# Optimization experiments

Measured on AMD Instinct MI355X. Metric: run time of the kernel, lower is better.

## Reference

```python
import jax, jax.numpy as jnp
import numpy as np

NEG_INF = -1e30


def setup_inputs() -> dict:
    key = jax.random.key(0)
    x = jax.random.normal(key, (8192, 128), dtype=jnp.float32)
    return {"x": x, "k": 16}


def reference(x, k):
    # L2-normalize rows (cosine geometry), matching x / x.norm(p=2, dim=1)
    xn = x / jnp.linalg.norm(x, axis=1, keepdims=True)
    # All-pairs similarity S[i, j] = x_i . x_j  -> [N, N]
    S = jnp.matmul(xn, xn.T)
    # Denominator in the original includes ALL entries (self included):
    # log(exp(S[i,j]) / sum_m exp(S[i,m])) = S[i,j] - logsumexp_m S[i,m]
    lse = jax.nn.logsumexp(S, axis=1)  # [N]
    # BallTree on L2-normalized vectors orders neighbors by cosine similarity;
    # query(k+1) then dropping column 0 (self) == top-k of S with diagonal masked.
    n = S.shape[0]
    S_masked = jnp.where(jnp.eye(n, dtype=bool), NEG_INF, S)
    top_vals, _ = jax.lax.top_k(S_masked, k)  # [N, k]
    # loss = -sum_i sum_{j in kNN(i)} log(exp(S_ij)/denom_i)
    loss = -jnp.sum(top_vals - lse[:, None])
    return loss
```

## Files before the change

kernel.cpp:

```cpp
#include <hip/hip_runtime.h>
#include <math.h>

#define N 8192
#define D 128
#define KSEL 16
#define CH 512
#define NC (N / CH)
#define BM 128
#define PH 8
#define CPC 4
#define NEG_INF_F (-1e30f)
#define LOG2E 1.44269504f
#define LN2 0.69314718f

typedef __attribute__((ext_vector_type(8))) short short8;
typedef __attribute__((ext_vector_type(4))) float f32x4;
typedef __attribute__((ext_vector_type(2))) unsigned short ush2;

static __device__ __forceinline__ unsigned short f2bf(float f) {
    unsigned u = __float_as_uint(f);
    u += 0x7FFF + ((u >> 16) & 1);
    return (unsigned short)(u >> 16);
}

static __device__ __forceinline__ float exp2_raw(float x) {
    float r;
    asm("v_exp_f32 %0, %1" : "=v"(r) : "v"(x));
    return r;
}

#define GLOAD_LDS(gsrc, ldst)                                                     \
    __builtin_amdgcn_global_load_lds(                                             \
        (const __attribute__((address_space(1))) unsigned int*)(const void*)(gsrc),\
        (__attribute__((address_space(3))) unsigned int*)(void*)(ldst), 16, 0, 0)

__global__ void k_normalize(const float* __restrict__ x,
                            unsigned short* __restrict__ xnA,
                            unsigned short* __restrict__ xnB,
                            float* __restrict__ out) {
    if (blockIdx.x == 0 && threadIdx.x == 0) out[0] = 0.f;
    int row = blockIdx.x * 4 + (threadIdx.x >> 6);
    int lane = threadIdx.x & 63;
    const float2* x2 = (const float2*)(x + (size_t)row * D);
    float2 a = x2[lane];
    float s = fmaf(a.x, a.x, a.y * a.y);
#pragma unroll
    for (int off = 32; off > 0; off >>= 1) s += __shfl_xor(s, off, 64);
    float inv = rsqrtf(s);
    ush2 hb, ha;
    hb.x = f2bf(a.x * inv);
    hb.y = f2bf(a.y * inv);
    ha.x = f2bf(a.x * inv * LOG2E);
    ha.y = f2bf(a.y * inv * LOG2E);
    *(ush2*)(xnB + (size_t)row * D + lane * 2) = hb;
    *(ush2*)(xnA + (size_t)row * D + lane * 2) = ha;
}

__global__ __launch_bounds__(256, 4) void k_tiles(const unsigned short* __restrict__ xnA,
                                                  const unsigned short* __restrict__ xnB,
                                                  float* __restrict__ cs,
                                                  float* __restrict__ ct) {
    __shared__ unsigned short Bsh[2][4][4][64][8];

    const int tid = threadIdx.x;
    const int w = tid >> 6;
    const int l = tid & 63;
    const int r = l & 15;
    const int p = l >> 4;
    const int i0 = blockIdx.x * BM;
    const int j0 = blockIdx.y * CH;
    const int by = blockIdx.y;

    const unsigned short* ap = xnA + (size_t)(i0 + w * 16 + r) * D + p * 8;
    short8 af0 = *(const short8*)(ap);
    short8 af1 = *(const short8*)(ap + 32);
    short8 af2 = *(const short8*)(ap + 64);
    short8 af3 = *(const short8*)(ap + 96);
    const unsigned short* gp = ap + (size_t)64 * D;
    short8 ag0 = *(const short8*)(gp);
    short8 ag1 = *(const short8*)(gp + 32);
    short8 ag2 = *(const short8*)(gp + 64);
    short8 ag3 = *(const short8*)(gp + 96);

    float sE[2][4], c0[2][4], c1[2][4];
#pragma unroll
    for (int s2 = 0; s2 < 2; ++s2)
#pragma unroll
        for (int q = 0; q < 4; ++q) {
            sE[s2][q] = 0.f;
            c0[s2][q] = c1[s2][q] = NEG_INF_F;
        }

    const unsigned short* sbase = xnB + (size_t)(j0 + r) * D + p * 8 + w * 32;

#pragma unroll
    for (int tt = 0; tt < 4; ++tt)
        GLOAD_LDS(sbase + (size_t)tt * (16 * D), &Bsh[0][tt][w][0][0]);
    __syncthreads();

    for (int ph = 0; ph < PH; ++ph) {
        const int buf = ph & 1;
        if (ph < PH - 1) {
            const unsigned short* s1 = sbase + (size_t)(ph + 1) * (64 * D);
#pragma unroll
            for (int tt = 0; tt < 4; ++tt)
                GLOAD_LDS(s1 + (size_t)tt * (16 * D), &Bsh[buf ^ 1][tt][w][0][0]);
        }
#pragma unroll
        for (int tt = 0; tt < 4; ++tt) {
            short8 b0 = *(const short8*)&Bsh[buf][tt][0][l][0];
            short8 b1 = *(const short8*)&Bsh[buf][tt][1][l][0];
            short8 b2 = *(const short8*)&Bsh[buf][tt][2][l][0];
            short8 b3 = *(const short8*)&Bsh[buf][tt][3][l][0];
            f32x4 a0 = {0.f, 0.f, 0.f, 0.f};
            f32x4 a1 = {0.f, 0.f, 0.f, 0.f};
            a0 = __builtin_amdgcn_mfma_f32_16x16x32_bf16(af0, b0, a0, 0, 0, 0);
            a0 = __builtin_amdgcn_mfma_f32_16x16x32_bf16(af1, b1, a0, 0, 0, 0);
            a0 = __builtin_amdgcn_mfma_f32_16x16x32_bf16(af2, b2, a0, 0, 0, 0);
            a0 = __builtin_amdgcn_mfma_f32_16x16x32_bf16(af3, b3, a0, 0, 0, 0);
            a1 = __builtin_amdgcn_mfma_f32_16x16x32_bf16(ag0, b0, a1, 0, 0, 0);
            a1 = __builtin_amdgcn_mfma_f32_16x16x32_bf16(ag1, b1, a1, 0, 0, 0);
            a1 = __builtin_amdgcn_mfma_f32_16x16x32_bf16(ag2, b2, a1, 0, 0, 0);
            a1 = __builtin_amdgcn_mfma_f32_16x16x32_bf16(ag3, b3, a1, 0, 0, 0);
#pragma unroll
            for (int q = 0; q < 4; ++q) {
                float v = a0[q];
                sE[0][q] += exp2_raw(v);
                float n0 = fmaxf(c0[0][q], v);
                c1[0][q] = __builtin_amdgcn_fmed3f(c0[0][q], c1[0][q], v);
                c0[0][q] = n0;
                v = a1[q];
                sE[1][q] += exp2_raw(v);
                n0 = fmaxf(c0[1][q], v);
                c1[1][q] = __builtin_amdgcn_fmed3f(c0[1][q], c1[1][q], v);
                c0[1][q] = n0;
            }
        }
        __syncthreads();
    }

#pragma unroll
    for (int s2 = 0; s2 < 2; ++s2) {
#pragma unroll
        for (int o = 1; o <= 4; o <<= 1) {
#pragma unroll
            for (int q = 0; q < 4; ++q) {
                float o0 = __shfl_xor(c0[s2][q], o, 64);
                float o1 = __shfl_xor(c1[s2][q], o, 64);
                float m0 = fminf(c0[s2][q], o0);
                c0[s2][q] = fmaxf(c0[s2][q], o0);
                c1[s2][q] = fmaxf(c1[s2][q], m0);
                c1[s2][q] = fmaxf(c1[s2][q], o1);
            }
        }
#pragma unroll
        for (int o = 1; o <= 8; o <<= 1)
#pragma unroll
            for (int q = 0; q < 4; ++q)
                sE[s2][q] += __shfl_xor(sE[s2][q], o, 64);

        const int rowbase = i0 + s2 * 64 + w * 16 + p * 4;
        if ((r & 7) == 0) {
            int rG = r >> 3;
#pragma unroll
            for (int q = 0; q < 4; ++q) {
                float2 v2 = make_float2(c0[s2][q], c1[s2][q]);
                *(float2*)(ct + (size_t)(rowbase + q) * (NC * CPC) + by * CPC + rG * 2) = v2;
            }
        }
        if (r == 0) {
#pragma unroll
            for (int q = 0; q < 4; ++q)
                cs[(size_t)(rowbase + q) * NC + by] = sE[s2][q];
        }
    }
}

__global__ __launch_bounds__(256) void k_merge(const float* __restrict__ cs,
                                               const float* __restrict__ ct,
                                               float* __restrict__ out) {
    __shared__ float sh[4];
    const int w = threadIdx.x >> 6, l = threadIdx.x & 63;
    const int row = blockIdx.x * 4 + w;

    float s = cs[(size_t)row * NC + (l & 15)];
#pragma unroll
    for (int o = 1; o <= 8; o <<= 1) s += __shfl_xor(s, o, 64);
    float lse = logf(s);

    float v = ct[(size_t)row * (NC * CPC) + l];
#pragma unroll
    for (int k = 2; k <= 64; k <<= 1) {
#pragma unroll
        for (int j = k >> 1; j > 0; j >>= 1) {
            float ov = __shfl_xor(v, j, 64);
            bool up = ((l & k) == 0);
            bool lower = ((l & j) == 0);
            float mn = fminf(v, ov), mx = fmaxf(v, ov);
            v = (up == lower) ? mx : mn;
        }
    }

    float t = (l >= 1 && l <= KSEL) ? v : 0.f;
#pragma unroll
    for (int o = 1; o <= 32; o <<= 1) t += __shfl_xor(t, o, 64);

    if (l == 0) sh[w] = (float)KSEL * lse - LN2 * t;
    __syncthreads();
    if (threadIdx.x == 0)
        atomicAdd(out, (sh[0] + sh[1]) + (sh[2] + sh[3]));
}

extern "C" void kernel_launch(void* const* d_in, const int* in_sizes, int n_in,
                              void* d_out, int out_size, void* d_ws, size_t ws_size,
                              hipStream_t stream) {
    const float* x = (const float*)d_in[0];
    float* out = (float*)d_out;

    unsigned short* xnA = (unsigned short*)d_ws;
    unsigned short* xnB = xnA + (size_t)N * D;
    float* cs = (float*)((char*)d_ws + (4u << 20));
    float* ct = cs + (size_t)N * NC;

    k_normalize<<<N / 4, 256, 0, stream>>>(x, xnA, xnB, out);
    k_tiles<<<dim3(N / BM, NC), 256, 0, stream>>>(xnA, xnB, cs, ct);
    k_merge<<<N / 4, 256, 0, stream>>>(cs, ct, out);
}
```

Measured before the change: 66.61 us.

## Fuse merge kernel into tile kernel via last-block atomic counter

Removes the separate merge kernel launch. Each row-block of the tile kernel bumps a per-row-block atomic counter, and the last column-chunk block to finish does the logsumexp and top-k merge for its 128 rows, then atomically adds to the output. This saves a launch and the gap between kernels, but the merge now runs serially in one block per row group, 32 rows per wave, after the tiles finish. It also adds fences and an atomic on every block.

```diff
diff --git a/kernel.cpp b/kernel.cpp
--- a/kernel.cpp
+++ b/kernel.cpp
@@ -37,8 +37,12 @@
 __global__ void k_normalize(const float* __restrict__ x,
                             unsigned short* __restrict__ xnA,
                             unsigned short* __restrict__ xnB,
+                            unsigned int* __restrict__ cnt,
                             float* __restrict__ out) {
-    if (blockIdx.x == 0 && threadIdx.x == 0) out[0] = 0.f;
+    if (blockIdx.x == 0) {
+        if (threadIdx.x == 0) out[0] = 0.f;
+        if (threadIdx.x < 64) cnt[threadIdx.x] = 0u;
+    }
     int row = blockIdx.x * 4 + (threadIdx.x >> 6);
     int lane = threadIdx.x & 63;
     const float2* x2 = (const float2*)(x + (size_t)row * D);
@@ -59,17 +63,22 @@
 __global__ __launch_bounds__(256, 4) void k_tiles(const unsigned short* __restrict__ xnA,
                                                   const unsigned short* __restrict__ xnB,
                                                   float* __restrict__ cs,
-                                                  float* __restrict__ ct) {
+                                                  float* __restrict__ ct,
+                                                  unsigned int* __restrict__ cnt,
+                                                  float* __restrict__ out) {
     __shared__ unsigned short Bsh[2][4][4][64][8];
+    __shared__ unsigned int lastFlag;
+    __shared__ float shf[4];
 
     const int tid = threadIdx.x;
     const int w = tid >> 6;
     const int l = tid & 63;
     const int r = l & 15;
     const int p = l >> 4;
-    const int i0 = blockIdx.x * BM;
-    const int j0 = blockIdx.y * CH;
+    const int bx = blockIdx.x;
     const int by = blockIdx.y;
+    const int i0 = bx * BM;
+    const int j0 = by * CH;
 
     const unsigned short* ap = xnA + (size_t)(i0 + w * 16 + r) * D + p * 8;
     short8 af0 = *(const short8*)(ap);
@@ -174,41 +183,48 @@
                 cs[(size_t)(rowbase + q) * NC + by] = sE[s2][q];
         }
     }
-}
-
-__global__ __launch_bounds__(256) void k_merge(const float* __restrict__ cs,
-                                               const float* __restrict__ ct,
-                                               float* __restrict__ out) {
-    __shared__ float sh[4];
-    const int w = threadIdx.x >> 6, l = threadIdx.x & 63;
-    const int row = blockIdx.x * 4 + w;
-
-    float s = cs[(size_t)row * NC + (l & 15)];
-#pragma unroll
-    for (int o = 1; o <= 8; o <<= 1) s += __shfl_xor(s, o, 64);
-    float lse = logf(s);
-
-    float v = ct[(size_t)row * (NC * CPC) + l];
-#pragma unroll
-    for (int k = 2; k <= 64; k <<= 1) {
-#pragma unroll
-        for (int j = k >> 1; j > 0; j >>= 1) {
-            float ov = __shfl_xor(v, j, 64);
-            bool up = ((l & k) == 0);
-            bool lower = ((l & j) == 0);
-            float mn = fminf(v, ov), mx = fmaxf(v, ov);
-            v = (up == lower) ? mx : mn;
-        }
-    }
-
-    float t = (l >= 1 && l <= KSEL) ? v : 0.f;
-#pragma unroll
-    for (int o = 1; o <= 32; o <<= 1) t += __shfl_xor(t, o, 64);
-
-    if (l == 0) sh[w] = (float)KSEL * lse - LN2 * t;
-    __syncthreads();
-    if (threadIdx.x == 0)
-        atomicAdd(out, (sh[0] + sh[1]) + (sh[2] + sh[3]));
+
+    __syncthreads();
+    __threadfence();
+    if (tid == 0)
+        lastFlag = (atomicAdd(&cnt[bx], 1u) == (unsigned)(NC - 1)) ? 1u : 0u;
+    __syncthreads();
+    if (lastFlag == 0) return;
+    __threadfence();
+
+    float part = 0.f;
+    for (int rr = 0; rr < BM / 4; ++rr) {
+        const int row = i0 + w * (BM / 4) + rr;
+
+        float s = cs[(size_t)row * NC + (l & 15)];
+#pragma unroll
+        for (int o = 1; o <= 8; o <<= 1) s += __shfl_xor(s, o, 64);
+        float lse = logf(s);
+
+        float v = ct[(size_t)row * (NC * CPC) + l];
+#pragma unroll
+        for (int k = 2; k <= 64; k <<= 1) {
+#pragma unroll
+            for (int j = k >> 1; j > 0; j >>= 1) {
+                float ov = __shfl_xor(v, j, 64);
+                bool up = ((l & k) == 0);
+                bool lower = ((l & j) == 0);
+                float mn = fminf(v, ov), mx = fmaxf(v, ov);
+                v = (up == lower) ? mx : mn;
+            }
+        }
+
+        float t = (l >= 1 && l <= KSEL) ? v : 0.f;
+#pragma unroll
+        for (int o = 1; o <= 32; o <<= 1) t += __shfl_xor(t, o, 64);
+
+        part += (float)KSEL * lse - LN2 * t;
+    }
+
+    if (l == 0) shf[w] = part;
+    __syncthreads();
+    if (tid == 0)
+        atomicAdd(out, (shf[0] + shf[1]) + (shf[2] + shf[3]));
 }
 
 extern "C" void kernel_launch(void* const* d_in, const int* in_sizes, int n_in,
@@ -221,8 +237,8 @@
     unsigned short* xnB = xnA + (size_t)N * D;
     float* cs = (float*)((char*)d_ws + (4u << 20));
     float* ct = cs + (size_t)N * NC;
-
-    k_normalize<<<N / 4, 256, 0, stream>>>(x, xnA, xnB, out);
-    k_tiles<<<dim3(N / BM, NC), 256, 0, stream>>>(xnA, xnB, cs, ct);
-    k_merge<<<N / 4, 256, 0, stream>>>(cs, ct, out);
-}
+    unsigned int* cnt = (unsigned int*)(ct + (size_t)N * NC * CPC);
+
+    k_normalize<<<N / 4, 256, 0, stream>>>(x, xnA, xnB, cnt, out);
+    k_tiles<<<dim3(N / BM, NC), 256, 0, stream>>>(xnA, xnB, cs, ct, cnt, out);
+}
```

Result: slower. 180.3 us (+170.7%).
